# Performance work log

Hardware: AMD Instinct MI355X
Metric: run time of the kernel (lower is better)

## Reference

```python
import jax, jax.numpy as jnp
import numpy as np

N_NODES = 50000
N_EDGES = 600000
DIM = 128
VOCAB = 512
PAD_ID = 0
LN_EPS = 1e-5


def setup_inputs() -> dict:
    key = jax.random.key(0)
    ks = jax.random.split(key, 8)
    node_ids = jax.random.randint(ks[0], (N_NODES,), 0, VOCAB, dtype=jnp.int32)
    edge_index = jax.random.randint(ks[1], (2, N_EDGES), 0, N_NODES, dtype=jnp.int32)
    edge_weight = jax.random.uniform(ks[2], (N_EDGES,), dtype=jnp.float32)
    # embedding with padding row zeroed (padding_idx semantics)
    emb = jax.random.normal(ks[3], (VOCAB, DIM), dtype=jnp.float32) * 0.05
    emb = emb.at[PAD_ID].set(0.0)
    s = 1.0 / np.sqrt(DIM)
    W1 = jax.random.normal(ks[4], (DIM, DIM), dtype=jnp.float32) * s
    b1 = jnp.zeros((DIM,), jnp.float32)
    W2 = jax.random.normal(ks[5], (DIM, DIM), dtype=jnp.float32) * s
    b2 = jnp.zeros((DIM,), jnp.float32)
    return {
        "node_ids": node_ids, "edge_index": edge_index, "edge_weight": edge_weight,
        "emb": emb, "W1": W1, "b1": b1, "W2": W2, "b2": b2,
        "gamma1": jnp.ones((DIM,), jnp.float32), "beta1": jnp.zeros((DIM,), jnp.float32),
        "gamma2": jnp.ones((DIM,), jnp.float32), "beta2": jnp.zeros((DIM,), jnp.float32),
    }


def _gcn_conv(x, row, col, ew, W, b, n_nodes):
    """PyG GCNConv: normalize=True, add_self_loops=True, improved=False.
    Aggregation j->i: edge (row=src j, col=dst i)."""
    h = x @ W  # [N, out]
    # add self loops with weight 1
    loop = jnp.arange(n_nodes, dtype=row.dtype)
    row_f = jnp.concatenate([row, loop])
    col_f = jnp.concatenate([col, loop])
    ew_f = jnp.concatenate([ew, jnp.ones((n_nodes,), ew.dtype)])
    # symmetric degree normalization (deg over destination index)
    deg = jax.ops.segment_sum(ew_f, col_f, num_segments=n_nodes)
    dis = jnp.where(deg > 0, jax.lax.rsqrt(jnp.maximum(deg, 1e-12)), 0.0)
    norm = dis[row_f] * ew_f * dis[col_f]  # [E+N]
    msg = norm[:, None] * h[row_f]  # gather + scale  [E+N, out]
    out = jax.ops.segment_sum(msg, col_f, num_segments=n_nodes)  # scatter-add
    return out + b


def _layer_norm(x, gamma, beta):
    mu = jnp.mean(x, axis=-1, keepdims=True)
    var = jnp.mean(jnp.square(x - mu), axis=-1, keepdims=True)
    return (x - mu) * jax.lax.rsqrt(var + LN_EPS) * gamma + beta


def reference(node_ids, edge_index, edge_weight, emb, W1, b1, W2, b2,
              gamma1, beta1, gamma2, beta2):
    row, col = edge_index[0], edge_index[1]
    x = emb[node_ids]  # [N, D]
    x1 = _gcn_conv(x, row, col, edge_weight, W1, b1, N_NODES)
    x = _layer_norm(x + x1, gamma1, beta1)  # dropout is identity in eval
    x2 = _gcn_conv(x, row, col, edge_weight, W2, b2, N_NODES)
    x = _layer_norm(x + x2, gamma2, beta2)
    return x
```

## Files before the change

kernel.cpp:

```cpp
#include <hip/hip_runtime.h>

#define N_NODES 50000
#define N_EDGES 600000
#define DIM     128
#define VOCAB   512
#define LN_EPS  1e-5f
#define FIXS    16777216.0f
#define BCAP    64

typedef unsigned int uint;
typedef unsigned long long ull;
typedef unsigned short ushort;
typedef unsigned char uchar;
typedef __attribute__((ext_vector_type(8))) short s8v;
typedef __attribute__((ext_vector_type(4))) float f4v;
typedef __attribute__((ext_vector_type(4))) int   i4v;
typedef __attribute__((ext_vector_type(4))) float fv4;
typedef __attribute__((ext_vector_type(2))) float f2v;

__device__ __forceinline__ uint f2bf(float f) {
    uint u = __float_as_uint(f);
    return (u + 0x7fffu + ((u >> 16) & 1u)) >> 16;
}
__device__ __forceinline__ float bf_lo(uint p) { return __uint_as_float(p << 16); }
__device__ __forceinline__ float bf_hi(uint p) { return __uint_as_float(p & 0xffff0000u); }
__device__ __forceinline__ float dis_of(ull pv) {
    return rsqrtf(1.0f + (float)(uint)(pv & 0xffffffffu) * (1.0f / FIXS));
}

__global__ __launch_bounds__(256) void deg_mm1_kernel(
        const int* __restrict__ ei, const float* __restrict__ ew,
        ull* pack, const int* __restrict__ nid, int2* __restrict__ epack, int E,
        const float* __restrict__ X, const float* __restrict__ W,
        uint* __restrict__ Hb, int M,
        const float* __restrict__ W2, ushort* __restrict__ Wp) {
    __shared__ float Wt[32 * 128];
    __shared__ float Xt[64 * 36];
    int tid = threadIdx.x;
    int nbDeg = (E / 4 + 255) / 256;
    int nmm = (M + 63) / 64;
    if ((int)blockIdx.x < nbDeg) {
        int e0 = (blockIdx.x * 256 + tid) * 4;
        if (e0 >= E) return;
        i4v s4 = __builtin_nontemporal_load((const i4v*)(ei + e0));
        i4v c4 = __builtin_nontemporal_load((const i4v*)(ei + E + e0));
        fv4 w4 = __builtin_nontemporal_load((const fv4*)(ew + e0));
        int   s[4] = {s4.x, s4.y, s4.z, s4.w};
        int   c[4] = {c4.x, c4.y, c4.z, c4.w};
        float w[4] = {w4.x, w4.y, w4.z, w4.w};
        int nv[4];
        #pragma unroll
        for (int k = 0; k < 4; k++) nv[k] = nid[s[k]];
        ull r[4];
        #pragma unroll
        for (int k = 0; k < 4; k++) {
            ull a = (1ull << 32) | (ull)(uint)__float2int_rn(w[k] * FIXS);
            r[k] = atomicAdd(&pack[c[k]], a);
        }
        #pragma unroll
        for (int k = 0; k < 4; k++) {
            int rk = (int)(uint)(r[k] >> 32);
            epack[(size_t)c[k] * BCAP + rk] =
                make_int2(s[k] | (nv[k] << 16), __float_as_int(w[k]));
        }
        return;
    }
    if ((int)blockIdx.x >= nbDeg + nmm) {
        int o = (blockIdx.x - nbDeg - nmm) * 256 + tid;
        int j = o & 7, lane = (o >> 3) & 63, chunk = o >> 9;
        int kc = chunk & 3, nc = chunk >> 2;
        int k = kc * 32 + (lane >> 4) * 8 + j;
        int n = nc * 16 + (lane & 15);
        Wp[o] = (ushort)f2bf(W2[k * 128 + n]);
        return;
    }
    int bx = blockIdx.x - nbDeg;
    int tx = tid & 31, ty = tid >> 5;
    int r0 = bx * 64;
    float acc[8][4];
    #pragma unroll
    for (int j = 0; j < 8; j++)
        #pragma unroll
        for (int c = 0; c < 4; c++) acc[j][c] = 0.f;

    for (int kb = 0; kb < 128; kb += 32) {
        __syncthreads();
        #pragma unroll
        for (int q = 0; q < 4; q++) {
            int f = q * 256 + tid;
            ((float4*)Wt)[f] = *(const float4*)(W + kb * 128 + f * 4);
        }
        #pragma unroll
        for (int q = 0; q < 2; q++) {
            int f = q * 256 + tid;
            int row = f >> 3, cs = f & 7;
            int gr = r0 + row;
            float4 xv = make_float4(0.f, 0.f, 0.f, 0.f);
            if (gr < M) xv = *(const float4*)(X + (size_t)gr * 128 + kb + cs * 4);
            *(float4*)(Xt + row * 36 + cs * 4) = xv;
        }
        __syncthreads();
        #pragma unroll
        for (int k = 0; k < 32; k += 4) {
            float wv[4][4];
            #pragma unroll
            for (int kk = 0; kk < 4; kk++) {
                float4 t4 = *(const float4*)(Wt + (k + kk) * 128 + tx * 4);
                wv[kk][0] = t4.x; wv[kk][1] = t4.y; wv[kk][2] = t4.z; wv[kk][3] = t4.w;
            }
            #pragma unroll
            for (int j = 0; j < 8; j++) {
                float4 xv = *(const float4*)(Xt + (ty * 8 + j) * 36 + k);
                float xs[4] = {xv.x, xv.y, xv.z, xv.w};
                #pragma unroll
                for (int kk = 0; kk < 4; kk++)
                    #pragma unroll
                    for (int c = 0; c < 4; c++)
                        acc[j][c] = fmaf(xs[kk], wv[kk][c], acc[j][c]);
            }
        }
    }
    #pragma unroll
    for (int j = 0; j < 8; j++) {
        int gr = r0 + ty * 8 + j;
        if (gr < M) {
            uint p0 = f2bf(acc[j][0]) | (f2bf(acc[j][1]) << 16);
            uint p1 = f2bf(acc[j][2]) | (f2bf(acc[j][3]) << 16);
            ((uint2*)Hb)[(size_t)gr * 32 + tx] = make_uint2(p0, p1);
        }
    }
}

__global__ __launch_bounds__(256) void mm2_mfma(const uint* __restrict__ Xb,
                                                const ushort* __restrict__ Wp,
                                                const ull* __restrict__ pack,
                                                char* __restrict__ H8,
                                                float* __restrict__ rowscale, int M) {
    int wid = (blockIdx.x * 256 + threadIdx.x) >> 6;
    int lane = threadIdx.x & 63;
    int r0 = wid * 16;
    if (r0 >= M) return;
    int quad = lane >> 4, lo = lane & 15;
    const uint* xrow = Xb + (size_t)(r0 + lo) * 64 + quad * 4;
    s8v a[4];
    #pragma unroll
    for (int kc = 0; kc < 4; kc++) a[kc] = *(const s8v*)(xrow + kc * 16);
    f4v acc[8];
    #pragma unroll
    for (int nc = 0; nc < 8; nc++) {
        acc[nc] = (f4v){0.f, 0.f, 0.f, 0.f};
        #pragma unroll
        for (int kc = 0; kc < 4; kc++) {
            s8v b = *(const s8v*)(Wp + (size_t)((nc * 4 + kc) * 64 + lane) * 8);
            acc[nc] = __builtin_amdgcn_mfma_f32_16x16x32_bf16(a[kc], b, acc[nc], 0, 0, 0);
        }
    }
    float m[4];
    #pragma unroll
    for (int r = 0; r < 4; r++) {
        m[r] = 0.f;
        #pragma unroll
        for (int nc = 0; nc < 8; nc++) m[r] = fmaxf(m[r], fabsf(acc[nc][r]));
    }
    #pragma unroll
    for (int o = 1; o <= 8; o <<= 1)
        #pragma unroll
        for (int r = 0; r < 4; r++) m[r] = fmaxf(m[r], __shfl_xor(m[r], o, 64));
    #pragma unroll
    for (int r = 0; r < 4; r++) {
        float inv = (m[r] > 0.f) ? 127.0f / m[r] : 0.f;
        if (lo == 0) {
            int rr = r0 + quad * 4 + r;
            rowscale[rr] = m[r] * (1.0f / 127.0f) * dis_of(pack[rr]);
        }
        char* hp = H8 + (size_t)(r0 + quad * 4 + r) * 128 + lo;
        #pragma unroll
        for (int nc = 0; nc < 8; nc++)
            hp[nc * 16] = (char)__float2int_rn(acc[nc][r] * inv);
    }
}

template<int SHIFT, bool RESID_BF, bool OUT_BF, bool GI8, bool EDGE_DIS>
__global__ __launch_bounds__(256) void agg_ln(const ull* __restrict__ pack,
                                              const int2* __restrict__ epack,
                                              const void* __restrict__ hb,
                                              const float* __restrict__ rowscale,
                                              const int* __restrict__ nid,
                                              const void* __restrict__ resid,
                                              const float* __restrict__ bias,
                                              const float* __restrict__ gamma,
                                              const float* __restrict__ beta,
                                              void* __restrict__ out, int n) {
    int i = (blockIdx.x * 256 + threadIdx.x) >> 6;
    int lane = threadIdx.x & 63;
    if (i >= n) return;
    int iw = __builtin_amdgcn_readfirstlane(i);
    ull pv = pack[iw];
    int deg = (int)(pv >> 32);
    float dl = dis_of(pv);
    int hri = nid ? nid[iw] : iw;
    float slo, shi;
    if (GI8) {
        uint ps = ((const ushort*)hb)[(size_t)hri * 64 + lane];
        float sc = rowscale[hri];
        slo = sc * (float)(signed char)(ps & 0xffu);
        shi = sc * (float)(signed char)(ps >> 8);
    } else {
        uint ps = ((const uint*)hb)[(size_t)hri * 64 + lane];
        slo = bf_lo(ps); shi = bf_hi(ps);
    }
    float sx[4] = {GI8 ? slo : dl * slo, 0.f, 0.f, 0.f};
    float sy[4] = {GI8 ? shi : dl * shi, 0.f, 0.f, 0.f};
    const int2* ep = epack + (size_t)iw * BCAP;
    for (int j = 0; j < deg; j += 8) {
        int2 er[8];
        #pragma unroll
        for (int k = 0; k < 8; k++) {
            int idx = (j + k < deg) ? j + k : deg - 1;
            er[k] = ep[idx];
        }
        uint qv[8];
        float sc[8];
        #pragma unroll
        for (int k = 0; k < 8; k++) {
            uint ex = (uint)er[k].x;
            size_t row = (ex >> SHIFT) & 0xffffu;
            if (GI8) {
                qv[k] = ((const ushort*)hb)[row * 64 + lane];
                sc[k] = rowscale[row];
            } else {
                qv[k] = ((const uint*)hb)[row * 64 + lane];
                if (EDGE_DIS)
                    sc[k] = (float)((const uint*)pack)[2 * (size_t)(ex & 0xffffu)];
            }
        }
        #pragma unroll
        for (int k = 0; k < 8; k++) {
            float w = (j + k < deg) ? __int_as_float(er[k].y) : 0.f;
            float lo, hi;
            if (GI8) {
                w *= sc[k];
                lo = (float)(signed char)(qv[k] & 0xffu);
                hi = (float)(signed char)(qv[k] >> 8);
            } else {
                if (EDGE_DIS) w *= rsqrtf(1.0f + sc[k] * (1.0f / FIXS));
                lo = bf_lo(qv[k]); hi = bf_hi(qv[k]);
            }
            sx[k & 3] += w * lo;
            sy[k & 3] += w * hi;
        }
    }
    float acc0 = (sx[0] + sx[1]) + (sx[2] + sx[3]);
    float acc1 = (sy[0] + sy[1]) + (sy[2] + sy[3]);
    float2 xr;
    if (RESID_BF) {
        uint pr = __builtin_nontemporal_load((const uint*)resid + (size_t)hri * 64 + lane);
        xr = make_float2(bf_lo(pr), bf_hi(pr));
    } else {
        xr = ((const float2*)resid)[(size_t)hri * 64 + lane];
    }
    float2 bi = ((const float2*)bias)[lane];
    float v0 = xr.x + dl * acc0 + bi.x;
    float v1 = xr.y + dl * acc1 + bi.y;
    float s1 = v0 + v1, s2 = v0 * v0 + v1 * v1;
    #pragma unroll
    for (int o = 32; o > 0; o >>= 1) {
        s1 += __shfl_xor(s1, o, 64);
        s2 += __shfl_xor(s2, o, 64);
    }
    float mu   = s1 * (1.0f / DIM);
    float var  = s2 * (1.0f / DIM) - mu * mu;
    float rstd = rsqrtf(var + LN_EPS);
    float2 ga = ((const float2*)gamma)[lane];
    float2 be = ((const float2*)beta)[lane];
    float o0 = (v0 - mu) * rstd * ga.x + be.x;
    float o1 = (v1 - mu) * rstd * ga.y + be.y;
    if (OUT_BF) {
        __builtin_nontemporal_store(f2bf(o0) | (f2bf(o1) << 16),
                                    (uint*)out + (size_t)i * 64 + lane);
    } else {
        f2v ov = {o0, o1};
        __builtin_nontemporal_store(ov, (f2v*)((float2*)out + (size_t)i * 64 + lane));
    }
}

extern "C" void kernel_launch(void* const* d_in, const int* in_sizes, int n_in,
                              void* d_out, int out_size, void* d_ws, size_t ws_size,
                              hipStream_t stream) {
    const int*   node_ids = (const int*)  d_in[0];
    const int*   ei       = (const int*)  d_in[1];
    const float* ew       = (const float*)d_in[2];
    const float* emb      = (const float*)d_in[3];
    const float* W1       = (const float*)d_in[4];
    const float* b1       = (const float*)d_in[5];
    const float* W2       = (const float*)d_in[6];
    const float* b2       = (const float*)d_in[7];
    const float* g1       = (const float*)d_in[8];
    const float* be1      = (const float*)d_in[9];
    const float* g2       = (const float*)d_in[10];
    const float* be2      = (const float*)d_in[11];
    float* out = (float*)d_out;

    char* p = (char*)d_ws;
    auto alloc = [&](size_t bytes) {
        char* r = p;
        p += (bytes + 255) & ~(size_t)255;
        return r;
    };
    char*   h8      = (char*)  alloc((size_t)N_NODES * DIM);
    float*  rsc     = (float*) alloc((size_t)N_NODES * 4);
    uint*   x1b     = (uint*)  alloc((size_t)N_NODES * 64 * 4);
    uint*   hembB   = (uint*)  alloc((size_t)VOCAB * 64 * 4);
    ushort* Wp      = (ushort*)alloc((size_t)128 * 128 * 2);
    ull*    pack    = (ull*)   alloc((size_t)N_NODES * 8);
    int2*   epack   = (int2*)  alloc((size_t)N_NODES * BCAP * 8);

    int nbDeg = (N_EDGES / 4 + 255) / 256;
    int nmm = (VOCAB + 63) / 64;

    (void)hipMemsetAsync(pack, 0, (size_t)N_NODES * 8, stream);
    deg_mm1_kernel<<<nbDeg + nmm + 64, 256, 0, stream>>>(
        ei, ew, pack, node_ids, epack, N_EDGES, emb, W1, hembB, VOCAB, W2, Wp);

    agg_ln<16, false, true, false, true><<<(N_NODES + 3) / 4, 256, 0, stream>>>(
        pack, epack, hembB, nullptr, node_ids, emb, b1, g1, be1, x1b, N_NODES);

    mm2_mfma<<<(N_NODES / 16 + 3) / 4, 256, 0, stream>>>(x1b, Wp, pack, h8, rsc, N_NODES);
    agg_ln<0, true, false, true, false><<<(N_NODES + 3) / 4, 256, 0, stream>>>(
        pack, epack, h8, rsc, nullptr, x1b, b2, g2, be2, out, N_NODES);
}
```

Before: 212.4 us.

## Pack degree and edges into 32-bit words with quantized edge weights

The per-node degree/weight-sum accumulator shrinks from 64-bit to 32-bit: the count sits in the top 6 bits and the weight sum is 20-bit fixed point. Edge records shrink from 8 to 4 bytes by storing the source index with a 16-bit quantized weight, and the node_id lookup moves from edge build into the first aggregation. This halves atomic and edge-list memory traffic. The cost is coarser weight precision and a hard limit of 63 in-degree entries per node before the count bits overflow.

Result: no change. 216.1 us (+1.8%).

```diff
diff --git a/kernel.cpp b/kernel.cpp
--- a/kernel.cpp
+++ b/kernel.cpp
@@ -5,13 +5,13 @@
 #define DIM     128
 #define VOCAB   512
 #define LN_EPS  1e-5f
-#define FIXS    16777216.0f
+#define FIX20   1048576.0f
+#define WSC     65535.0f
 #define BCAP    64
 
 typedef unsigned int uint;
 typedef unsigned long long ull;
 typedef unsigned short ushort;
-typedef unsigned char uchar;
 typedef __attribute__((ext_vector_type(8))) short s8v;
 typedef __attribute__((ext_vector_type(4))) float f4v;
 typedef __attribute__((ext_vector_type(4))) int   i4v;
@@ -24,13 +24,13 @@
 }
 __device__ __forceinline__ float bf_lo(uint p) { return __uint_as_float(p << 16); }
 __device__ __forceinline__ float bf_hi(uint p) { return __uint_as_float(p & 0xffff0000u); }
-__device__ __forceinline__ float dis_of(ull pv) {
-    return rsqrtf(1.0f + (float)(uint)(pv & 0xffffffffu) * (1.0f / FIXS));
+__device__ __forceinline__ float dis_of(uint pv) {
+    return rsqrtf(1.0f + (float)(pv & 0x03ffffffu) * (1.0f / FIX20));
 }
 
 __global__ __launch_bounds__(256) void deg_mm1_kernel(
         const int* __restrict__ ei, const float* __restrict__ ew,
-        ull* pack, const int* __restrict__ nid, int2* __restrict__ epack, int E,
+        uint* pack, uint* __restrict__ epack, int E,
         const float* __restrict__ X, const float* __restrict__ W,
         uint* __restrict__ Hb, int M,
         const float* __restrict__ W2, ushort* __restrict__ Wp) {
@@ -48,20 +48,17 @@
         int   s[4] = {s4.x, s4.y, s4.z, s4.w};
         int   c[4] = {c4.x, c4.y, c4.z, c4.w};
         float w[4] = {w4.x, w4.y, w4.z, w4.w};
-        int nv[4];
-        #pragma unroll
-        for (int k = 0; k < 4; k++) nv[k] = nid[s[k]];
-        ull r[4];
+        uint r[4];
         #pragma unroll
         for (int k = 0; k < 4; k++) {
-            ull a = (1ull << 32) | (ull)(uint)__float2int_rn(w[k] * FIXS);
+            uint a = (1u << 26) | (uint)__float2int_rn(w[k] * FIX20);
             r[k] = atomicAdd(&pack[c[k]], a);
         }
         #pragma unroll
         for (int k = 0; k < 4; k++) {
-            int rk = (int)(uint)(r[k] >> 32);
-            epack[(size_t)c[k] * BCAP + rk] =
-                make_int2(s[k] | (nv[k] << 16), __float_as_int(w[k]));
+            uint rk = r[k] >> 26;
+            uint wq = (uint)__float2int_rn(w[k] * WSC);
+            epack[(size_t)c[k] * BCAP + rk] = (uint)s[k] | (wq << 16);
         }
         return;
     }
@@ -133,7 +130,7 @@
 
 __global__ __launch_bounds__(256) void mm2_mfma(const uint* __restrict__ Xb,
                                                 const ushort* __restrict__ Wp,
-                                                const ull* __restrict__ pack,
+                                                const uint* __restrict__ pack,
                                                 char* __restrict__ H8,
                                                 float* __restrict__ rowscale, int M) {
     int wid = (blockIdx.x * 256 + threadIdx.x) >> 6;
@@ -180,9 +177,9 @@
     }
 }
 
-template<int SHIFT, bool RESID_BF, bool OUT_BF, bool GI8, bool EDGE_DIS>
-__global__ __launch_bounds__(256) void agg_ln(const ull* __restrict__ pack,
-                                              const int2* __restrict__ epack,
+template<bool RESID_BF, bool OUT_BF, bool GI8>
+__global__ __launch_bounds__(256) void agg_ln(const uint* __restrict__ pack,
+                                              const uint* __restrict__ epack,
                                               const void* __restrict__ hb,
                                               const float* __restrict__ rowscale,
                                               const int* __restrict__ nid,
@@ -195,10 +192,10 @@
     int lane = threadIdx.x & 63;
     if (i >= n) return;
     int iw = __builtin_amdgcn_readfirstlane(i);
-    ull pv = pack[iw];
-    int deg = (int)(pv >> 32);
+    uint pv = pack[iw];
+    int deg = (int)(pv >> 26);
     float dl = dis_of(pv);
-    int hri = nid ? nid[iw] : iw;
+    int hri = GI8 ? iw : nid[iw];
     float slo, shi;
     if (GI8) {
         uint ps = ((const ushort*)hb)[(size_t)hri * 64 + lane];
@@ -211,9 +208,9 @@
     }
     float sx[4] = {GI8 ? slo : dl * slo, 0.f, 0.f, 0.f};
     float sy[4] = {GI8 ? shi : dl * shi, 0.f, 0.f, 0.f};
-    const int2* ep = epack + (size_t)iw * BCAP;
+    const uint* ep = epack + (size_t)iw * BCAP;
     for (int j = 0; j < deg; j += 8) {
-        int2 er[8];
+        uint er[8];
         #pragma unroll
         for (int k = 0; k < 8; k++) {
             int idx = (j + k < deg) ? j + k : deg - 1;
@@ -223,27 +220,26 @@
         float sc[8];
         #pragma unroll
         for (int k = 0; k < 8; k++) {
-            uint ex = (uint)er[k].x;
-            size_t row = (ex >> SHIFT) & 0xffffu;
+            uint src = er[k] & 0xffffu;
             if (GI8) {
-                qv[k] = ((const ushort*)hb)[row * 64 + lane];
-                sc[k] = rowscale[row];
+                qv[k] = ((const ushort*)hb)[(size_t)src * 64 + lane];
+                sc[k] = rowscale[src];
             } else {
+                size_t row = (uint)nid[src];
                 qv[k] = ((const uint*)hb)[row * 64 + lane];
-                if (EDGE_DIS)
-                    sc[k] = (float)((const uint*)pack)[2 * (size_t)(ex & 0xffffu)];
+                sc[k] = (float)(pack[src] & 0x03ffffffu);
             }
         }
         #pragma unroll
         for (int k = 0; k < 8; k++) {
-            float w = (j + k < deg) ? __int_as_float(er[k].y) : 0.f;
+            float w = (j + k < deg) ? (float)(er[k] >> 16) * (1.0f / WSC) : 0.f;
             float lo, hi;
             if (GI8) {
                 w *= sc[k];
                 lo = (float)(signed char)(qv[k] & 0xffu);
                 hi = (float)(signed char)(qv[k] >> 8);
             } else {
-                if (EDGE_DIS) w *= rsqrtf(1.0f + sc[k] * (1.0f / FIXS));
+                w *= rsqrtf(1.0f + sc[k] * (1.0f / FIX20));
                 lo = bf_lo(qv[k]); hi = bf_hi(qv[k]);
             }
             sx[k & 3] += w * lo;
@@ -312,20 +308,20 @@
     uint*   x1b     = (uint*)  alloc((size_t)N_NODES * 64 * 4);
     uint*   hembB   = (uint*)  alloc((size_t)VOCAB * 64 * 4);
     ushort* Wp      = (ushort*)alloc((size_t)128 * 128 * 2);
-    ull*    pack    = (ull*)   alloc((size_t)N_NODES * 8);
-    int2*   epack   = (int2*)  alloc((size_t)N_NODES * BCAP * 8);
+    uint*   pack    = (uint*)  alloc((size_t)N_NODES * 4);
+    uint*   epack   = (uint*)  alloc((size_t)N_NODES * BCAP * 4);
 
     int nbDeg = (N_EDGES / 4 + 255) / 256;
     int nmm = (VOCAB + 63) / 64;
 
-    (void)hipMemsetAsync(pack, 0, (size_t)N_NODES * 8, stream);
+    (void)hipMemsetAsync(pack, 0, (size_t)N_NODES * 4, stream);
     deg_mm1_kernel<<<nbDeg + nmm + 64, 256, 0, stream>>>(
-        ei, ew, pack, node_ids, epack, N_EDGES, emb, W1, hembB, VOCAB, W2, Wp);
-
-    agg_ln<16, false, true, false, true><<<(N_NODES + 3) / 4, 256, 0, stream>>>(
+        ei, ew, pack, epack, N_EDGES, emb, W1, hembB, VOCAB, W2, Wp);
+
+    agg_ln<false, true, false><<<(N_NODES + 3) / 4, 256, 0, stream>>>(
         pack, epack, hembB, nullptr, node_ids, emb, b1, g1, be1, x1b, N_NODES);
 
     mm2_mfma<<<(N_NODES / 16 + 3) / 4, 256, 0, stream>>>(x1b, Wp, pack, h8, rsc, N_NODES);
-    agg_ln<0, true, false, true, false><<<(N_NODES + 3) / 4, 256, 0, stream>>>(
+    agg_ln<true, false, true><<<(N_NODES + 3) / 4, 256, 0, stream>>>(
         pack, epack, h8, rsc, nullptr, x1b, b2, g2, be2, out, N_NODES);
 }
```
